# Optimization experiments

Measured on AMD Instinct MI355X. Metric: run time of the kernel, lower is better.

The kernel has to match this reference:

```python
import jax, jax.numpy as jnp
import numpy as np

B, T, C = 2, 2048, 1024
N = 16
D = C // N  # 64


def setup_inputs() -> dict:
    key = jax.random.key(0)
    ks = jax.random.split(key, 5)
    s = 1.0 / np.sqrt(C)  # lecun_normal-ish scale for Dense kernels
    return {
        "src": jax.random.normal(ks[0], (B, T, C), jnp.float32),
        "mask": jnp.ones((B, T), jnp.float32),  # unused on causal path
        "Wq": jax.random.normal(ks[1], (C, C), jnp.float32) * s,
        "bq": jnp.zeros((C,), jnp.float32),
        "Wk": jax.random.normal(ks[2], (C, C), jnp.float32) * s,
        "bk": jnp.zeros((C,), jnp.float32),
        "Wv": jax.random.normal(ks[3], (C, C), jnp.float32) * s,
        "bv": jnp.zeros((C,), jnp.float32),
        "Wo": jax.random.normal(ks[4], (C, C), jnp.float32) * s,
        "bo": jnp.zeros((C,), jnp.float32),
    }


def reference(src, mask, Wq, bq, Wk, bk, Wv, bv, Wo, bo):
    # QKV projections -> [B, N, T, D]
    def heads(x):
        return x.reshape(B, T, N, D).transpose(0, 2, 1, 3)

    q = heads(src @ Wq + bq)
    k = heads(src @ Wk + bk)
    v = heads(src @ Wv + bv)

    # scores [B, N, T, T], causal mask, softmax
    scores = jnp.einsum("bntd,bnsd->bnts", q, k) / jnp.sqrt(jnp.float32(D))
    causal = jnp.tril(jnp.ones((T, T), bool))
    scores = jnp.where(causal, scores, -jnp.inf)
    attn = jax.nn.softmax(scores, axis=-1)

    # weighted values, merge heads, output projection (dropout deterministic)
    out = jnp.einsum("bnts,bnsd->bntd", attn, v)
    out = out.transpose(0, 2, 1, 3).reshape(B, T, C)
    return out @ Wo + bo
```

## Files before the change

### kernel.cpp

```cpp
#include <hip/hip_runtime.h>

typedef __bf16 bf16;
typedef bf16 bf16x8 __attribute__((ext_vector_type(8)));
typedef float f32x4 __attribute__((ext_vector_type(4)));
typedef unsigned short u16;
typedef u16 u16x4 __attribute__((ext_vector_type(4)));
typedef u16 u16x8 __attribute__((ext_vector_type(8)));

typedef const __attribute__((address_space(1))) void* gptr_t;
typedef __attribute__((address_space(3))) void* sptr_t;

__device__ __forceinline__ void async16(const void* g, void* l) {
  __builtin_amdgcn_global_load_lds((gptr_t)g, (sptr_t)l, 16, 0, 0);
}
__device__ __forceinline__ u16 f2bf(float v) {
  return __builtin_bit_cast(u16, (bf16)v);
}

__device__ __forceinline__ size_t paddr(int r, int k, int KT) {
  return (size_t)((r >> 4) * KT + (k >> 5)) * 512 + ((k >> 3) & 3) * 128 +
         (r & 15) * 8 + (k & 7);
}

__global__ void kPrep(const float* __restrict__ src, u16* __restrict__ Xp,
                      const float* __restrict__ Wq, const float* __restrict__ Wk,
                      const float* __restrict__ Wv, const float* __restrict__ Wo,
                      u16* __restrict__ Wp) {
  __shared__ float tile[32][33];
  const int bid = blockIdx.x, tid = threadIdx.x;
  if (bid < 4096) {
    const int i = (bid * 256 + tid) * 4;
    const int m = i >> 10, k = i & 1023;
    float4 v = *(const float4*)&src[i];
    u16x4 o = {f2bf(v.x), f2bf(v.y), f2bf(v.z), f2bf(v.w)};
    *(u16x4*)&Xp[paddr(m, k, 32)] = o;
  } else {
    const int t = bid - 4096;
    const int z = t >> 10, tt = t & 1023;
    const float* W = (z == 0) ? Wq : (z == 1) ? Wk : (z == 2) ? Wv : Wo;
    const int n0 = (tt & 31) * 32, k0 = (tt >> 5) * 32;
    const int tx = tid & 31, ty = tid >> 5;
#pragma unroll
    for (int j = 0; j < 4; ++j)
      tile[ty + j * 8][tx] = W[(size_t)(k0 + ty + j * 8) * 1024 + n0 + tx];
    __syncthreads();
    if (tid < 128) {
      const int sub = tid >> 6, l = tid & 63, hi = l >> 4, lo = l & 15;
      u16x8 o;
#pragma unroll
      for (int e = 0; e < 8; ++e) o[e] = f2bf(tile[hi * 8 + e][sub * 16 + lo]);
      const size_t ad = (size_t)z * 1048576 +
                        (size_t)(((n0 >> 4) + sub) * 32 + (k0 >> 5)) * 512 +
                        hi * 128 + lo * 8;
      *(u16x8*)&Wp[ad] = o;
    }
  }
}

__global__ __launch_bounds__(256, 3) void kGemmQKV(
    const u16* __restrict__ A, const u16* __restrict__ Bt,
    const float* __restrict__ b0, const float* __restrict__ b1,
    const float* __restrict__ b2, u16* __restrict__ outQ) {
  __shared__ __align__(16) u16 Als[2][16 * 512];
  const int tid = threadIdx.x, l = tid & 63, w = tid >> 6;
  const int bid = (blockIdx.x & 7) * 96 + (blockIdx.x >> 3);
  const int mb = bid & 31, nb = bid >> 5;
  const int mbase = mb * 128, nbase = nb * 128;
  const int wr = (w >> 1) * 64, wc = (w & 1) * 64;
  const int hi = l >> 4, lo = l & 15;

  const u16* bb[4];
#pragma unroll
  for (int nf = 0; nf < 4; ++nf)
    bb[nf] = &Bt[(size_t)((nbase + wc + nf * 16) >> 4) * 16384 + l * 8];

  f32x4 acc[4][4];
#pragma unroll
  for (int i = 0; i < 4; ++i)
#pragma unroll
    for (int j = 0; j < 4; ++j) acc[i][j] = (f32x4){0.f, 0.f, 0.f, 0.f};

  auto stageW = [&](int bufi, int u) {
#pragma unroll
    for (int i = 0; i < 4; ++i) {
      const int f = w * 4 + i;
      const int fr = f >> 1, kk = f & 1;
      async16(&A[(size_t)((mb * 8 + fr) * 32 + 2 * u + kk) * 512 + l * 8],
              &Als[bufi][f * 512]);
    }
  };

  bf16x8 bw0[2][4], bw1[2][4];
  stageW(0, 0);
#pragma unroll
  for (int kk = 0; kk < 2; ++kk)
#pragma unroll
    for (int nf = 0; nf < 4; ++nf)
      bw0[kk][nf] = *(const bf16x8*)&bb[nf][kk * 512];

  auto window = [&](int u, bf16x8 (&bc)[2][4], bf16x8 (&bn)[2][4]) {
    const int cur = u & 1;
    if (u < 15) {
      stageW(cur ^ 1, u + 1);
#pragma unroll
      for (int kk = 0; kk < 2; ++kk)
#pragma unroll
        for (int nf = 0; nf < 4; ++nf)
          bn[kk][nf] = *(const bf16x8*)&bb[nf][(2 * (u + 1) + kk) * 512];
      asm volatile("s_waitcnt vmcnt(12)" ::: "memory");
    } else {
      asm volatile("s_waitcnt vmcnt(0)" ::: "memory");
    }
    __builtin_amdgcn_s_barrier();
    __builtin_amdgcn_sched_barrier(0);

#pragma unroll
    for (int kk = 0; kk < 2; ++kk) {
      bf16x8 a[4];
#pragma unroll
      for (int mf = 0; mf < 4; ++mf)
        a[mf] = *(const bf16x8*)&Als[cur][((((w >> 1) * 4 + mf) * 2) + kk) * 512 +
                                          l * 8];
#pragma unroll
      for (int mf = 0; mf < 4; ++mf)
#pragma unroll
        for (int nf = 0; nf < 4; ++nf)
          acc[mf][nf] = __builtin_amdgcn_mfma_f32_16x16x32_bf16(a[mf], bc[kk][nf],
                                                                acc[mf][nf], 0, 0, 0);
    }
    __builtin_amdgcn_s_barrier();
  };

  for (int u2 = 0; u2 < 16; u2 += 2) {
    window(u2, bw0, bw1);
    window(u2 + 1, bw1, bw0);
  }

  u16* Qo = outQ;
  u16* Ko = outQ + 4 * 1048576;
  u16* Vo = outQ + 8 * 1048576;
  const int mat = nb >> 3;
  const float* bias = (mat == 0) ? b0 : (mat == 1) ? b1 : b2;
  const float qs = (mat == 0) ? 0.1803368801f : 1.0f;
#pragma unroll
  for (int nf = 0; nf < 4; ++nf) {
    const int n = nbase + wc + nf * 16 + lo;
    const int cc = n & 1023, h = cc >> 6, d = cc & 63;
    const float bsv = bias[cc];
#pragma unroll
    for (int mf = 0; mf < 4; ++mf)
#pragma unroll
      for (int r = 0; r < 4; ++r) {
        const int m = mbase + wr + mf * 16 + hi * 4 + r;
        const int bb_ = m >> 11, t = m & 2047;
        const u16 hv = f2bf((acc[mf][nf][r] + bsv) * qs);
        const size_t hd = (size_t)(bb_ * 16 + h) * 131072;
        if (mat < 2) {
          (mat == 0 ? Qo : Ko)[hd + paddr(t, d, 2)] = hv;
        } else {
          Vo[hd + paddr(d, t, 64)] = hv;
        }
      }
  }
}

__global__ __launch_bounds__(256, 2) void kGemmO(
    const u16* __restrict__ A, const u16* __restrict__ Bt,
    const float* __restrict__ b0, float* __restrict__ outF) {
  __shared__ __align__(16) u16 Als[2][16 * 512];
  const int tid = threadIdx.x, l = tid & 63, w = tid >> 6;
  const int bid = (blockIdx.x & 7) * 64 + (blockIdx.x >> 3);
  const int mb = bid & 31, nb = bid >> 5;
  const int mbase = mb * 128, nbase = nb * 64;
  const int wr = (w >> 1) * 64, wc = (w & 1) * 32;
  const int hi = l >> 4, lo = l & 15;

  const u16* bb[2];
#pragma unroll
  for (int nf = 0; nf < 2; ++nf)
    bb[nf] = &Bt[(size_t)((nbase + wc + nf * 16) >> 4) * 16384 + l * 8];

  f32x4 acc[4][2];
#pragma unroll
  for (int i = 0; i < 4; ++i)
#pragma unroll
    for (int j = 0; j < 2; ++j) acc[i][j] = (f32x4){0.f, 0.f, 0.f, 0.f};

  auto stageW = [&](int bufi, int u) {
#pragma unroll
    for (int i = 0; i < 4; ++i) {
      const int f = w * 4 + i;
      const int fr = f >> 1, kk = f & 1;
      async16(&A[(size_t)((mb * 8 + fr) * 32 + 2 * u + kk) * 512 + l * 8],
              &Als[bufi][f * 512]);
    }
  };

  bf16x8 bw0[2][2], bw1[2][2];
  stageW(0, 0);
#pragma unroll
  for (int kk = 0; kk < 2; ++kk)
#pragma unroll
    for (int nf = 0; nf < 2; ++nf)
      bw0[kk][nf] = *(const bf16x8*)&bb[nf][kk * 512];

  auto window = [&](int u, bf16x8 (&bc)[2][2], bf16x8 (&bn)[2][2]) {
    const int cur = u & 1;
    if (u < 15) {
      stageW(cur ^ 1, u + 1);
#pragma unroll
      for (int kk = 0; kk < 2; ++kk)
#pragma unroll
        for (int nf = 0; nf < 2; ++nf)
          bn[kk][nf] = *(const bf16x8*)&bb[nf][(2 * (u + 1) + kk) * 512];
      asm volatile("s_waitcnt vmcnt(8)" ::: "memory");
    } else {
      asm volatile("s_waitcnt vmcnt(0)" ::: "memory");
    }
    __builtin_amdgcn_s_barrier();
    __builtin_amdgcn_sched_barrier(0);

#pragma unroll
    for (int kk = 0; kk < 2; ++kk) {
      bf16x8 a[4];
#pragma unroll
      for (int mf = 0; mf < 4; ++mf)
        a[mf] = *(const bf16x8*)&Als[cur][((((w >> 1) * 4 + mf) * 2) + kk) * 512 +
                                          l * 8];
#pragma unroll
      for (int mf = 0; mf < 4; ++mf)
#pragma unroll
        for (int nf = 0; nf < 2; ++nf)
          acc[mf][nf] = __builtin_amdgcn_mfma_f32_16x16x32_bf16(a[mf], bc[kk][nf],
                                                                acc[mf][nf], 0, 0, 0);
    }
    __builtin_amdgcn_s_barrier();
  };

  for (int u2 = 0; u2 < 16; u2 += 2) {
    window(u2, bw0, bw1);
    window(u2 + 1, bw1, bw0);
  }

#pragma unroll
  for (int nf = 0; nf < 2; ++nf) {
    const int n = nbase + wc + nf * 16 + lo;
    const float bsv = b0[n];
#pragma unroll
    for (int mf = 0; mf < 4; ++mf)
#pragma unroll
      for (int r = 0; r < 4; ++r) {
        const int m = mbase + wr + mf * 16 + hi * 4 + r;
        outF[(size_t)m * 1024 + n] = acc[mf][nf][r] + bsv;
      }
  }
}

#define PSTR 36
__global__ __launch_bounds__(512, 2) void kAttn(const u16* __restrict__ Qp,
                                                const u16* __restrict__ Kp,
                                                const u16* __restrict__ Vp,
                                                u16* __restrict__ AOp) {
  __shared__ __align__(16) u16 Pl[8][16 * PSTR];
  __shared__ __align__(16) float Red[4][2][16][64];
  __shared__ float RedL[4][2][64];
  const int tid = threadIdx.x, l = tid & 63, w = tid >> 6;
  const int grp = w >> 1, half = w & 1;
  const int g = l >> 4, c = l & 15;
  const int id = blockIdx.x;
  const int xcd = id & 7, rem = id >> 3;
  const int pi = rem & 7, bh = (rem >> 3) * 8 + xcd;
  const int qt0 = 31 - pi, qt1 = 16 + pi, qt2 = 15 - pi, qt3 = pi;
  const size_t head = (size_t)bh * 131072;
  const u16* Kh = Kp + head;
  const u16* Vh = Vp + head;

  bf16x8 aq0[2], aq1[2], aq2[2], aq3[2];
#pragma unroll
  for (int ks = 0; ks < 2; ++ks) {
    aq0[ks] = *(const bf16x8*)&Qp[head + (size_t)((qt0 * 4 + grp) * 2 + ks) * 512 + l * 8];
    aq1[ks] = *(const bf16x8*)&Qp[head + (size_t)((qt1 * 4 + grp) * 2 + ks) * 512 + l * 8];
    aq2[ks] = *(const bf16x8*)&Qp[head + (size_t)((qt2 * 4 + grp) * 2 + ks) * 512 + l * 8];
    aq3[ks] = *(const bf16x8*)&Qp[head + (size_t)((qt3 * 4 + grp) * 2 + ks) * 512 + l * 8];
  }

  f32x4 acc0[4], acc1[4], acc2[4], acc3[4];
#pragma unroll
  for (int i = 0; i < 4; ++i) {
    acc0[i] = (f32x4){0.f, 0.f, 0.f, 0.f};
    acc1[i] = (f32x4){0.f, 0.f, 0.f, 0.f};
    acc2[i] = (f32x4){0.f, 0.f, 0.f, 0.f};
    acc3[i] = (f32x4){0.f, 0.f, 0.f, 0.f};
  }
  float l0 = 0.f, l1 = 0.f, l2 = 0.f, l3 = 0.f;

  bf16x8 kr[4];
#pragma unroll
  for (int f = 0; f < 4; ++f)
    kr[f] = *(const bf16x8*)&Kh[(size_t)((half * 2 + (f >> 1)) * 2 + (f & 1)) * 512 + l * 8];
  bf16x8 vr[4];

  auto qkTile = [&](const bf16x8* aq, f32x4* sT) {
#pragma unroll
    for (int sf = 0; sf < 2; ++sf)
#pragma unroll
      for (int ks = 0; ks < 2; ++ks)
        sT[sf] = __builtin_amdgcn_mfma_f32_16x16x32_bf16(kr[sf * 2 + ks], aq[ks],
                                                         sT[sf], 0, 0, 0);
  };

  auto finishTile = [&](const f32x4* sT, bool diag, f32x4* accO, float& lpart) {
    float v[8];
#pragma unroll
    for (int sf = 0; sf < 2; ++sf)
#pragma unroll
      for (int r = 0; r < 4; ++r) v[sf * 4 + r] = sT[sf][r];
    if (diag) {
      const int qin = grp * 16 + c;
#pragma unroll
      for (int sf = 0; sf < 2; ++sf)
#pragma unroll
        for (int r = 0; r < 4; ++r)
          if (half * 32 + sf * 16 + g * 4 + r > qin) v[sf * 4 + r] = -__builtin_inff();
    }
    float p[8];
#pragma unroll
    for (int i = 0; i < 8; ++i) p[i] = __builtin_exp2f(v[i]);
#pragma unroll
    for (int sf = 0; sf < 2; ++sf) {
      u16x4 q4 = {f2bf(p[sf * 4 + 0]), f2bf(p[sf * 4 + 1]),
                  f2bf(p[sf * 4 + 2]), f2bf(p[sf * 4 + 3])};
      *(u16x4*)&Pl[w][c * PSTR + sf * 16 + g * 4] = q4;
    }
    lpart += ((p[0] + p[1]) + (p[2] + p[3])) + ((p[4] + p[5]) + (p[6] + p[7]));
    bf16x8 pf = *(const bf16x8*)&Pl[w][c * PSTR + g * 8];
#pragma unroll
    for (int nd = 0; nd < 4; ++nd)
      accO[nd] = __builtin_amdgcn_mfma_f32_16x16x32_bf16(pf, vr[nd], accO[nd], 0, 0, 0);
  };

  const int nst = qt0 + 1;
  for (int st = 0; st < nst; ++st) {
#pragma unroll
    for (int nd = 0; nd < 4; ++nd)
      vr[nd] = *(const bf16x8*)&Vh[(size_t)(nd * 64 + st * 2 + half) * 512 + l * 8];

    f32x4 sT[2];
    if (st <= qt3) {
#pragma unroll
      for (int i = 0; i < 2; ++i) sT[i] = (f32x4){0.f, 0.f, 0.f, 0.f};
      qkTile(aq3, sT);
      finishTile(sT, st == qt3, acc3, l3);
    }
    if (st <= qt2) {
#pragma unroll
      for (int i = 0; i < 2; ++i) sT[i] = (f32x4){0.f, 0.f, 0.f, 0.f};
      qkTile(aq2, sT);
      finishTile(sT, st == qt2, acc2, l2);
    }
    if (st <= qt1) {
#pragma unroll
      for (int i = 0; i < 2; ++i) sT[i] = (f32x4){0.f, 0.f, 0.f, 0.f};
      qkTile(aq1, sT);
      finishTile(sT, st == qt1, acc1, l1);
    }
    {
#pragma unroll
      for (int i = 0; i < 2; ++i) sT[i] = (f32x4){0.f, 0.f, 0.f, 0.f};
      qkTile(aq0, sT);
      if (st < qt0) {
#pragma unroll
        for (int f = 0; f < 4; ++f)
          kr[f] = *(const bf16x8*)&Kh[(size_t)(((st + 1) * 4 + half * 2 + (f >> 1)) * 2 +
                                               (f & 1)) * 512 + l * 8];
      }
      finishTile(sT, st == qt0, acc0, l0);
    }
  }

  const int b = bh >> 4, h = bh & 15;
  auto writeOut = [&](int qt, const f32x4* accO, float lc) {
#pragma unroll
    for (int r = 0; r < 4; ++r) {
      const float lr = __shfl(lc, g * 4 + r);
      const float rin = 1.0f / lr;
      const int mg = b * 2048 + qt * 64 + grp * 16 + g * 4 + r;
#pragma unroll
      for (int nd = 0; nd < 4; ++nd) {
        const int col = h * 64 + nd * 16 + c;
        AOp[paddr(mg, col, 32)] = f2bf(accO[nd][r] * rin);
      }
    }
  };
  auto combinePair = [&](f32x4* accX, float lX, int qtX, f32x4* accY, float lY,
                         int qtY) {
    float lcX = lX + __shfl_xor(lX, 16);
    lcX += __shfl_xor(lcX, 32);
    float lcY = lY + __shfl_xor(lY, 16);
    lcY += __shfl_xor(lcY, 32);
    __syncthreads();
    if (half) {
#pragma unroll
      for (int nd = 0; nd < 4; ++nd)
#pragma unroll
        for (int r = 0; r < 4; ++r) {
          Red[grp][0][nd * 4 + r][l] = accX[nd][r];
          Red[grp][1][nd * 4 + r][l] = accY[nd][r];
        }
      RedL[grp][0][l] = lcX;
      RedL[grp][1][l] = lcY;
    }
    __syncthreads();
    if (!half) {
#pragma unroll
      for (int nd = 0; nd < 4; ++nd)
#pragma unroll
        for (int r = 0; r < 4; ++r) {
          accX[nd][r] += Red[grp][0][nd * 4 + r][l];
          accY[nd][r] += Red[grp][1][nd * 4 + r][l];
        }
      writeOut(qtX, accX, lcX + RedL[grp][0][l]);
      writeOut(qtY, accY, lcY + RedL[grp][1][l]);
    }
  };
  combinePair(acc0, l0, qt0, acc1, l1, qt1);
  combinePair(acc2, l2, qt2, acc3, l3, qt3);
}

extern "C" void kernel_launch(void* const* d_in, const int* in_sizes, int n_in,
                              void* d_out, int out_size, void* d_ws, size_t ws_size,
                              hipStream_t stream) {
  const float* src = (const float*)d_in[0];
  const float* Wq = (const float*)d_in[2];
  const float* bq = (const float*)d_in[3];
  const float* Wk = (const float*)d_in[4];
  const float* bk = (const float*)d_in[5];
  const float* Wv = (const float*)d_in[6];
  const float* bv = (const float*)d_in[7];
  const float* Wo = (const float*)d_in[8];
  const float* bo = (const float*)d_in[9];
  float* out = (float*)d_out;

  char* ws = (char*)d_ws;
  u16* Wp = (u16*)(ws);
  u16* Xp = (u16*)(ws + 8ull * 1024 * 1024);
  u16* Qb = (u16*)(ws + 16ull * 1024 * 1024);
  u16* AOp = (u16*)(ws + 40ull * 1024 * 1024);

  kPrep<<<dim3(8192), dim3(256), 0, stream>>>(src, Xp, Wq, Wk, Wv, Wo, Wp);
  kGemmQKV<<<dim3(768), dim3(256), 0, stream>>>(Xp, Wp, bq, bk, bv, Qb);
  kAttn<<<dim3(256), dim3(512), 0, stream>>>(Qb, Qb + 4 * 1048576,
                                             Qb + 8 * 1048576, AOp);
  kGemmO<<<dim3(512), dim3(256), 0, stream>>>(AOp, Wp + 3ull * 1048576, bo, out);
}
```

Measured before the change: 111.9 us.

## Split GEMM B-register prefetch per k-half and raise priority around attention MFMAs

The QKV and output projection GEMM main loops now prefetch B fragments one k-half at a time, holding a two-slot register buffer instead of two full double-buffered sets. Each window waits only for the half it is about to consume, with adjusted vmcnt thresholds. This cuts register pressure and lets the next B loads overlap the current half's MFMAs. The attention kernel also wraps its QK and PV MFMA blocks in s_setprio(1)/s_setprio(0) so waves issuing matrix ops get scheduling priority over waves doing softmax work.

```diff
diff --git a/kernel.cpp b/kernel.cpp
--- a/kernel.cpp
+++ b/kernel.cpp
@@ -90,50 +90,53 @@
     }
   };
 
-  bf16x8 bw0[2][4], bw1[2][4];
+  auto mfmaHalf = [&](int cur, int kk, bf16x8 (&bc)[4]) {
+    bf16x8 a[4];
+#pragma unroll
+    for (int mf = 0; mf < 4; ++mf) {
+      const int fr = (w >> 1) * 4 + mf;
+      a[mf] = *(const bf16x8*)&Als[cur][(fr * 2 + kk) * 512 + l * 8];
+    }
+#pragma unroll
+    for (int mf = 0; mf < 4; ++mf)
+#pragma unroll
+      for (int nf = 0; nf < 4; ++nf)
+        acc[mf][nf] = __builtin_amdgcn_mfma_f32_16x16x32_bf16(a[mf], bc[nf],
+                                                              acc[mf][nf], 0, 0, 0);
+  };
+
+  bf16x8 breg[2][4];
+#pragma unroll
+  for (int nf = 0; nf < 4; ++nf) breg[0][nf] = *(const bf16x8*)&bb[nf][0];
   stageW(0, 0);
-#pragma unroll
-  for (int kk = 0; kk < 2; ++kk)
+
+  for (int u = 0; u < 16; ++u) {
+    const int cur = u & 1;
 #pragma unroll
     for (int nf = 0; nf < 4; ++nf)
-      bw0[kk][nf] = *(const bf16x8*)&bb[nf][kk * 512];
-
-  auto window = [&](int u, bf16x8 (&bc)[2][4], bf16x8 (&bn)[2][4]) {
-    const int cur = u & 1;
+      breg[1][nf] = *(const bf16x8*)&bb[nf][(2 * u + 1) * 512];
     if (u < 15) {
       stageW(cur ^ 1, u + 1);
-#pragma unroll
-      for (int kk = 0; kk < 2; ++kk)
-#pragma unroll
-        for (int nf = 0; nf < 4; ++nf)
-          bn[kk][nf] = *(const bf16x8*)&bb[nf][(2 * (u + 1) + kk) * 512];
-      asm volatile("s_waitcnt vmcnt(12)" ::: "memory");
+      asm volatile("s_waitcnt vmcnt(8)" ::: "memory");
+    } else {
+      asm volatile("s_waitcnt vmcnt(4)" ::: "memory");
+    }
+    __builtin_amdgcn_s_barrier();
+    __builtin_amdgcn_sched_barrier(0);
+    mfmaHalf(cur, 0, breg[0]);
+
+    if (u < 15) {
+#pragma unroll
+      for (int nf = 0; nf < 4; ++nf)
+        breg[0][nf] = *(const bf16x8*)&bb[nf][(2 * u + 2) * 512];
+      asm volatile("s_waitcnt vmcnt(8)" ::: "memory");
     } else {
       asm volatile("s_waitcnt vmcnt(0)" ::: "memory");
     }
+    __builtin_amdgcn_sched_barrier(0);
+    mfmaHalf(cur, 1, breg[1]);
     __builtin_amdgcn_s_barrier();
     __builtin_amdgcn_sched_barrier(0);
-
-#pragma unroll
-    for (int kk = 0; kk < 2; ++kk) {
-      bf16x8 a[4];
-#pragma unroll
-      for (int mf = 0; mf < 4; ++mf)
-        a[mf] = *(const bf16x8*)&Als[cur][((((w >> 1) * 4 + mf) * 2) + kk) * 512 +
-                                          l * 8];
-#pragma unroll
-      for (int mf = 0; mf < 4; ++mf)
-#pragma unroll
-        for (int nf = 0; nf < 4; ++nf)
-          acc[mf][nf] = __builtin_amdgcn_mfma_f32_16x16x32_bf16(a[mf], bc[kk][nf],
-                                                                acc[mf][nf], 0, 0, 0);
-    }
-    __builtin_amdgcn_s_barrier();
-  };
-
-  for (int u2 = 0; u2 < 16; u2 += 2) {
-    window(u2, bw0, bw1);
-    window(u2 + 1, bw1, bw0);
   }
 
   u16* Qo = outQ;
@@ -196,50 +199,53 @@
     }
   };
 
-  bf16x8 bw0[2][2], bw1[2][2];
+  auto mfmaHalf = [&](int cur, int kk, bf16x8 (&bc)[2]) {
+    bf16x8 a[4];
+#pragma unroll
+    for (int mf = 0; mf < 4; ++mf) {
+      const int fr = (w >> 1) * 4 + mf;
+      a[mf] = *(const bf16x8*)&Als[cur][(fr * 2 + kk) * 512 + l * 8];
+    }
+#pragma unroll
+    for (int mf = 0; mf < 4; ++mf)
+#pragma unroll
+      for (int nf = 0; nf < 2; ++nf)
+        acc[mf][nf] = __builtin_amdgcn_mfma_f32_16x16x32_bf16(a[mf], bc[nf],
+                                                              acc[mf][nf], 0, 0, 0);
+  };
+
+  bf16x8 breg[2][2];
+#pragma unroll
+  for (int nf = 0; nf < 2; ++nf) breg[0][nf] = *(const bf16x8*)&bb[nf][0];
   stageW(0, 0);
-#pragma unroll
-  for (int kk = 0; kk < 2; ++kk)
+
+  for (int u = 0; u < 16; ++u) {
+    const int cur = u & 1;
 #pragma unroll
     for (int nf = 0; nf < 2; ++nf)
-      bw0[kk][nf] = *(const bf16x8*)&bb[nf][kk * 512];
-
-  auto window = [&](int u, bf16x8 (&bc)[2][2], bf16x8 (&bn)[2][2]) {
-    const int cur = u & 1;
+      breg[1][nf] = *(const bf16x8*)&bb[nf][(2 * u + 1) * 512];
     if (u < 15) {
       stageW(cur ^ 1, u + 1);
-#pragma unroll
-      for (int kk = 0; kk < 2; ++kk)
-#pragma unroll
-        for (int nf = 0; nf < 2; ++nf)
-          bn[kk][nf] = *(const bf16x8*)&bb[nf][(2 * (u + 1) + kk) * 512];
-      asm volatile("s_waitcnt vmcnt(8)" ::: "memory");
+      asm volatile("s_waitcnt vmcnt(6)" ::: "memory");
+    } else {
+      asm volatile("s_waitcnt vmcnt(2)" ::: "memory");
+    }
+    __builtin_amdgcn_s_barrier();
+    __builtin_amdgcn_sched_barrier(0);
+    mfmaHalf(cur, 0, breg[0]);
+
+    if (u < 15) {
+#pragma unroll
+      for (int nf = 0; nf < 2; ++nf)
+        breg[0][nf] = *(const bf16x8*)&bb[nf][(2 * u + 2) * 512];
+      asm volatile("s_waitcnt vmcnt(6)" ::: "memory");
     } else {
       asm volatile("s_waitcnt vmcnt(0)" ::: "memory");
     }
+    __builtin_amdgcn_sched_barrier(0);
+    mfmaHalf(cur, 1, breg[1]);
     __builtin_amdgcn_s_barrier();
     __builtin_amdgcn_sched_barrier(0);
-
-#pragma unroll
-    for (int kk = 0; kk < 2; ++kk) {
-      bf16x8 a[4];
-#pragma unroll
-      for (int mf = 0; mf < 4; ++mf)
-        a[mf] = *(const bf16x8*)&Als[cur][((((w >> 1) * 4 + mf) * 2) + kk) * 512 +
-                                          l * 8];
-#pragma unroll
-      for (int mf = 0; mf < 4; ++mf)
-#pragma unroll
-        for (int nf = 0; nf < 2; ++nf)
-          acc[mf][nf] = __builtin_amdgcn_mfma_f32_16x16x32_bf16(a[mf], bc[kk][nf],
-                                                                acc[mf][nf], 0, 0, 0);
-    }
-    __builtin_amdgcn_s_barrier();
-  };
-
-  for (int u2 = 0; u2 < 16; u2 += 2) {
-    window(u2, bw0, bw1);
-    window(u2 + 1, bw1, bw0);
   }
 
 #pragma unroll
@@ -301,12 +307,14 @@
   bf16x8 vr[4];
 
   auto qkTile = [&](const bf16x8* aq, f32x4* sT) {
+    __builtin_amdgcn_s_setprio(1);
 #pragma unroll
     for (int sf = 0; sf < 2; ++sf)
 #pragma unroll
       for (int ks = 0; ks < 2; ++ks)
         sT[sf] = __builtin_amdgcn_mfma_f32_16x16x32_bf16(kr[sf * 2 + ks], aq[ks],
                                                          sT[sf], 0, 0, 0);
+    __builtin_amdgcn_s_setprio(0);
   };
 
   auto finishTile = [&](const f32x4* sT, bool diag, f32x4* accO, float& lpart) {
@@ -334,9 +342,11 @@
     }
     lpart += ((p[0] + p[1]) + (p[2] + p[3])) + ((p[4] + p[5]) + (p[6] + p[7]));
     bf16x8 pf = *(const bf16x8*)&Pl[w][c * PSTR + g * 8];
+    __builtin_amdgcn_s_setprio(1);
 #pragma unroll
     for (int nd = 0; nd < 4; ++nd)
       accO[nd] = __builtin_amdgcn_mfma_f32_16x16x32_bf16(pf, vr[nd], accO[nd], 0, 0, 0);
+    __builtin_amdgcn_s_setprio(0);
   };
 
   const int nst = qt0 + 1;
```

Result: faster. 103.7 us (-7.4%).
